# Kernel tuning notes

Hardware: AMD Instinct MI355X
Metric: run time of the kernel (lower is better)

The kernel has to match this reference:

```python
import jax, jax.numpy as jnp
import numpy as np

B, L, D, H = 2, 2048, 512, 8
DH = D // H
THRESHOLD = 0.1


def setup_inputs() -> dict:
    key = jax.random.key(0)
    ks = jax.random.split(key, 8)
    s = 0.02  # weight scale to keep activations sane
    return {
        "q_x": jax.random.normal(ks[0], (B, L, D), jnp.float32),
        "k_x": jax.random.normal(ks[1], (B, L, D), jnp.float32),
        "v_x": jax.random.normal(ks[2], (B, L, D), jnp.float32),
        "energy_coeffs": jax.random.normal(ks[3], (B, L, 16), jnp.float32),
        "Wq": jax.random.normal(ks[4], (D, D), jnp.float32) * s,
        "bq": jnp.zeros((D,), jnp.float32),
        "Wk": jax.random.normal(ks[5], (D, D), jnp.float32) * s,
        "bk": jnp.zeros((D,), jnp.float32),
        "Wv": jax.random.normal(ks[6], (D, D), jnp.float32) * s,
        "bv": jnp.zeros((D,), jnp.float32),
        "Wo": jax.random.normal(ks[7], (D, D), jnp.float32) * s,
        "bo": jnp.zeros((D,), jnp.float32),
    }


def reference(q_x, k_x, v_x, energy_coeffs, Wq, bq, Wk, bk, Wv, bv, Wo, bo):
    b, l, d = q_x.shape
    # QKV projections (torch Linear: x @ W.T + b), split heads -> [B,H,L,Dh]
    Q = (q_x @ Wq.T + bq).reshape(b, l, H, DH).transpose(0, 2, 1, 3)
    K = (k_x @ Wk.T + bk).reshape(b, -1, H, DH).transpose(0, 2, 1, 3)
    V = (v_x @ Wv.T + bv).reshape(b, -1, H, DH).transpose(0, 2, 1, 3)
    scores = jnp.einsum("bhqd,bhkd->bhqk", Q, K) / jnp.sqrt(jnp.float32(DH))
    # straight-through energy-based key mask
    energy = jnp.abs(energy_coeffs).mean(axis=-1)  # [B, Lk]
    soft = jax.nn.sigmoid((energy - THRESHOLD) * 10.0)
    hard = (energy > THRESHOLD).astype(q_x.dtype)
    mask_val = soft + jax.lax.stop_gradient(hard - soft)  # fwd=hard, grad=soft
    scores = scores + (1.0 - mask_val)[:, None, None, :] * (-1e9)
    attn = jax.nn.softmax(scores, axis=-1)
    out = jnp.einsum("bhqk,bhkd->bhqd", attn, V)
    out = out.transpose(0, 2, 1, 3).reshape(b, l, d)
    return out @ Wo.T + bo
```

## Files before the change

kernel.cpp:

```cpp
#include <hip/hip_runtime.h>
#include <stdint.h>

#define B_ 2
#define L_ 2048
#define D_ 512
#define H_ 8
#define DH_ 64

using frag8 = __attribute__((ext_vector_type(8))) short;
using bf4   = __attribute__((ext_vector_type(4))) short;
using f32x4 = __attribute__((ext_vector_type(4))) float;
using u32x4 = __attribute__((ext_vector_type(4))) unsigned int;

#define QSC 0.18033688011112042f

__device__ __forceinline__ unsigned short f2bf(float f) {
    unsigned int u = __float_as_uint(f);
    u += 0x7fffu + ((u >> 16) & 1u);
    return (unsigned short)(u >> 16);
}

__device__ __forceinline__ unsigned int cvtpk(float lo, float hi_) {
    unsigned int r;
    asm("v_cvt_pk_bf16_f32 %0, %1, %2" : "=v"(r) : "v"(lo), "v"(hi_));
    return r;
}

__device__ __forceinline__ void gl2lds16(const void* g, void* lds) {
    __builtin_amdgcn_global_load_lds((const __attribute__((address_space(1))) void*)g,
                                     (__attribute__((address_space(3))) void*)lds,
                                     16, 0, 0);
}

template<int N>
__device__ __forceinline__ void vmwait() {
    asm volatile("s_waitcnt vmcnt(%0)" :: "n"(N) : "memory");
}

__global__ __launch_bounds__(256) void cvt_mask_kernel(
    const float* __restrict__ qx, const float* __restrict__ kx, const float* __restrict__ vx,
    const float* __restrict__ Wq, const float* __restrict__ Wk, const float* __restrict__ Wv,
    const float* __restrict__ Wo, const float* __restrict__ ec,
    unsigned short* qb, unsigned short* kb, unsigned short* vb,
    unsigned short* wqb, unsigned short* wkb, unsigned short* wvb, unsigned short* wob,
    float* __restrict__ mk)
{
    const long NA = (long)B_ * L_ * D_;
    const long NW = (long)D_ * D_;
    const long total4 = (3 * NA + 4 * NW) / 4;
    long q4 = (long)blockIdx.x * 256 + threadIdx.x;
    if (q4 < total4) {
        long i = q4 * 4;
        const float* src; unsigned short* dst; long off;
        if (i < NA)            { src = qx; dst = qb; off = i; }
        else if (i < 2 * NA)   { src = kx; dst = kb; off = i - NA; }
        else if (i < 3 * NA)   { src = vx; dst = vb; off = i - 2 * NA; }
        else {
            long j = i - 3 * NA;
            int w = (int)(j / NW);
            off = j - (long)w * NW;
            src = (w == 0) ? Wq : (w == 1) ? Wk : (w == 2) ? Wv : Wo;
            dst = (w == 0) ? wqb : (w == 1) ? wkb : (w == 2) ? wvb : wob;
        }
        float4 v = *(const float4*)(src + off);
        ushort4 o;
        o.x = f2bf(v.x); o.y = f2bf(v.y); o.z = f2bf(v.z); o.w = f2bf(v.w);
        *(ushort4*)(dst + off) = o;
    } else {
        long i = q4 - total4;
        if (i < B_ * L_) {
            const float4* p4 = (const float4*)(ec + i * 16);
            float s = 0.0f;
#pragma unroll
            for (int j = 0; j < 4; ++j) {
                float4 v = p4[j];
                s += fabsf(v.x) + fabsf(v.y) + fabsf(v.z) + fabsf(v.w);
            }
            float energy = s * (1.0f / 16.0f);
            mk[i] = (energy > 0.1f) ? 0.0f : -1.0e9f;
        }
    }
}

struct GemmArgs { const unsigned short* A; const unsigned short* W;
                  const float* bias; void* C; int mode; };

template<int BM, int BN>
__global__ __launch_bounds__(256) void gemm_kernel(GemmArgs a0, GemmArgs a1, GemmArgs a2,
                                                   int M, int N, int K)
{
    const int nwg = gridDim.x * gridDim.y * gridDim.z;
    int flat = blockIdx.x + gridDim.x * (blockIdx.y + gridDim.y * blockIdx.z);
    int swz  = (flat & 7) * (nwg >> 3) + (flat >> 3);
    const int bx = swz % gridDim.x;
    int t2 = swz / gridDim.x;
    const int by = t2 % gridDim.y;
    const int bz = t2 / gridDim.y;

    GemmArgs ga = bz == 0 ? a0 : (bz == 1 ? a1 : a2);
    const unsigned short* __restrict__ A = ga.A;
    const unsigned short* __restrict__ W = ga.W;
    const float* __restrict__ bias = ga.bias;

    constexpr int MF = BM / 32;
    constexpr int NF = BN / 32;
    constexpr int NL = BM / 32 + BN / 32;

    __shared__ __align__(16) unsigned short As[2][BM * 64];
    __shared__ __align__(16) unsigned short Bs[2][BN * 64];

    const int tid  = threadIdx.x;
    const int lane = tid & 63;
    const int wave = tid >> 6;
    const int hi   = lane >> 4;
    const int ln   = lane & 15;
    const int wr   = wave >> 1;
    const int wc   = wave & 1;

    const long mBase = (long)by * BM;
    const long nBase = (long)bx * BN;

    f32x4 acc[MF][NF];
#pragma unroll
    for (int m = 0; m < MF; ++m)
#pragma unroll
        for (int n = 0; n < NF; ++n) acc[m][n] = (f32x4){0.f, 0.f, 0.f, 0.f};

#define GSTAGE(KT, BUF) do {                                                    \
    _Pragma("unroll")                                                           \
    for (int i_ = 0; i_ < BM / 32; ++i_) {                                      \
        int cl_ = i_ * 256 + tid;                                               \
        int r_ = cl_ >> 3, c_ = cl_ & 7, s_ = c_ ^ (r_ & 7);                    \
        gl2lds16(A + (mBase + r_) * K + (KT) + s_ * 8, As[BUF] + cl_ * 8);      \
    }                                                                           \
    _Pragma("unroll")                                                           \
    for (int i_ = 0; i_ < BN / 32; ++i_) {                                      \
        int cl_ = i_ * 256 + tid;                                               \
        int r_ = cl_ >> 3, c_ = cl_ & 7, s_ = c_ ^ (r_ & 7);                    \
        gl2lds16(W + (nBase + r_) * K + (KT) + s_ * 8, Bs[BUF] + cl_ * 8);      \
    }                                                                           \
} while (0)

    GSTAGE(0, 0);

    const int nk = K / 64;
    for (int t = 0; t < nk; ++t) {
        const int buf = t & 1;
        if (t + 1 < nk) {
            GSTAGE((t + 1) * 64, buf ^ 1);
            vmwait<NL>();
        } else {
            vmwait<0>();
        }
        __builtin_amdgcn_s_barrier();
        __builtin_amdgcn_sched_barrier(0);

        frag8 af[2][MF], bfr[2][NF];
#pragma unroll
        for (int kk = 0; kk < 2; ++kk) {
#pragma unroll
            for (int m = 0; m < MF; ++m) {
                int row = wr * (BM / 2) + m * 16 + ln;
                int c = (kk * 4 + hi) ^ (row & 7);
                af[kk][m] = *(const frag8*)(As[buf] + row * 64 + c * 8);
            }
#pragma unroll
            for (int n = 0; n < NF; ++n) {
                int row = wc * (BN / 2) + n * 16 + ln;
                int c = (kk * 4 + hi) ^ (row & 7);
                bfr[kk][n] = *(const frag8*)(Bs[buf] + row * 64 + c * 8);
            }
        }
        __builtin_amdgcn_s_setprio(1);
#pragma unroll
        for (int kk = 0; kk < 2; ++kk)
#pragma unroll
            for (int m = 0; m < MF; ++m)
#pragma unroll
                for (int n = 0; n < NF; ++n)
                    acc[m][n] = __builtin_amdgcn_mfma_f32_16x16x32_bf16(af[kk][m], bfr[kk][n], acc[m][n], 0, 0, 0);
        __builtin_amdgcn_s_setprio(0);
        __builtin_amdgcn_sched_barrier(0);
        __builtin_amdgcn_s_barrier();
    }
#undef GSTAGE

    const int mode = ga.mode;
#pragma unroll
    for (int m = 0; m < MF; ++m) {
#pragma unroll
        for (int n = 0; n < NF; ++n) {
            long col = nBase + wc * (BN / 2) + n * 16 + ln;
            float bv = bias[col];
#pragma unroll
            for (int j = 0; j < 4; ++j) {
                long row = mBase + wr * (BM / 2) + m * 16 + hi * 4 + j;
                float v = acc[m][n][j] + bv;
                if (mode == 3) {
                    ((float*)ga.C)[row * N + col] = v;
                } else if (mode == 2) {
                    int dh = (int)col & 63;
                    int swv = ((dh & 7) << 1) | ((dh >> 3) & 1);
                    long nt = (row & ~63L) | (long)(((((int)(row >> 2)) & 15) ^ swv) << 2) | (row & 3);
                    ((unsigned short*)ga.C)[col * (long)(B_ * L_) + nt] = f2bf(v);
                } else {
                    if (mode == 1) v *= QSC;
                    ((unsigned short*)ga.C)[row * N + col] = f2bf(v);
                }
            }
        }
    }
}

__global__ __launch_bounds__(512, 4) void attn_kernel(
    const unsigned short* __restrict__ Qg, const unsigned short* __restrict__ Kg,
    const unsigned short* __restrict__ Vt, const float* __restrict__ mkg,
    unsigned short* __restrict__ Og)
{
    const int tid  = threadIdx.x;
    const int lane = tid & 63;
    const int wave = tid >> 6;
    const int grp  = wave >> 2;
    const int wq   = wave & 3;
    const int gtid = tid & 255;
    const int hi   = lane >> 4;
    const int ln   = lane & 15;

    const int bh = blockIdx.y;
    const int b  = bh >> 3, h = bh & 7;
    const unsigned short* Qb = Qg + ((long)b * L_) * D_ + h * DH_;
    const unsigned short* Kb = Kg + ((long)b * L_) * D_ + h * DH_;
    const unsigned short* Vb = Vt + (long)(h * DH_) * (B_ * L_) + (long)b * L_;
    const float* mkb = mkg + (long)b * L_;

    __shared__ __align__(16) char smem[65536];
    unsigned short* KsG = (unsigned short*)(smem + grp * 32768);
    unsigned short* VsG = (unsigned short*)(smem + grp * 32768 + 16384);

    const int q0 = blockIdx.x * 64 + wq * 16;

    frag8 qf[2];
#pragma unroll
    for (int ks = 0; ks < 2; ++ks)
        qf[ks] = *(const frag8*)(Qb + (long)(q0 + ln) * D_ + ks * 32 + hi * 8);

    const int sw  = ((ln & 7) << 1) | ((ln >> 3) & 1);
    const int sl0 = ((hi     ) ^ sw) << 2;
    const int sl1 = ((hi + 4 ) ^ sw) << 2;
    const int sl2 = ((hi + 8 ) ^ sw) << 2;
    const int sl3 = ((hi + 12) ^ sw) << 2;

#define STAGE(TT, BUF) do {                                                     \
    _Pragma("unroll")                                                           \
    for (int c2_ = 0; c2_ < 2; ++c2_) {                                         \
        int cl_ = c2_ * 256 + gtid;                                             \
        int r_ = cl_ >> 3, c_ = cl_ & 7;                                        \
        gl2lds16(Kb + (long)((TT) * 64 + r_) * D_ + ((c_ ^ (r_ & 7)) << 3),     \
                 KsG + (BUF) * 4096 + cl_ * 8);                                 \
        gl2lds16(Vb + (long)r_ * (B_ * L_) + (TT) * 64 + (c_ << 3),             \
                 VsG + (BUF) * 4096 + cl_ * 8);                                 \
    }                                                                           \
} while (0)

    STAGE(grp, 0);

    f32x4 o[4];
#pragma unroll
    for (int g = 0; g < 4; ++g) o[g] = (f32x4){0.f, 0.f, 0.f, 0.f};
    float m_run = -__builtin_inff();
    float l_run = 0.0f;

    for (int i = 0; i < 16; ++i) {
        const int T = 2 * i + grp;
        const int buf = i & 1;

        float4 m40 = *(const float4*)(mkb + T * 64 +      4 * hi);
        float4 m41 = *(const float4*)(mkb + T * 64 + 16 + 4 * hi);
        float4 m42 = *(const float4*)(mkb + T * 64 + 32 + 4 * hi);
        float4 m43 = *(const float4*)(mkb + T * 64 + 48 + 4 * hi);
        __builtin_amdgcn_sched_barrier(0);

        if (i < 15) {
            STAGE(2 * (i + 1) + grp, buf ^ 1);
            vmwait<8>();
        } else {
            vmwait<4>();
        }
        __builtin_amdgcn_s_barrier();
        __builtin_amdgcn_sched_barrier(0);

        const unsigned short* Kl = KsG + buf * 4096;
        const unsigned short* Vl = VsG + buf * 4096;

        f32x4 sv[4];
#pragma unroll
        for (int sh = 0; sh < 4; ++sh) sv[sh] = (f32x4){0.f, 0.f, 0.f, 0.f};
        __builtin_amdgcn_s_setprio(1);
#pragma unroll
        for (int sh = 0; sh < 4; ++sh) {
            int key = sh * 16 + ln;
#pragma unroll
            for (int ks = 0; ks < 2; ++ks) {
                frag8 kf = *(const frag8*)(Kl + key * 64 + (((ks * 4 + hi) ^ (ln & 7)) << 3));
                sv[sh] = __builtin_amdgcn_mfma_f32_16x16x32_bf16(kf, qf[ks], sv[sh], 0, 0, 0);
            }
        }
        __builtin_amdgcn_s_setprio(0);

        float sc[16];
        sc[0]  = sv[0][0] + m40.x; sc[1]  = sv[0][1] + m40.y;
        sc[2]  = sv[0][2] + m40.z; sc[3]  = sv[0][3] + m40.w;
        sc[4]  = sv[1][0] + m41.x; sc[5]  = sv[1][1] + m41.y;
        sc[6]  = sv[1][2] + m41.z; sc[7]  = sv[1][3] + m41.w;
        sc[8]  = sv[2][0] + m42.x; sc[9]  = sv[2][1] + m42.y;
        sc[10] = sv[2][2] + m42.z; sc[11] = sv[2][3] + m42.w;
        sc[12] = sv[3][0] + m43.x; sc[13] = sv[3][1] + m43.y;
        sc[14] = sv[3][2] + m43.z; sc[15] = sv[3][3] + m43.w;

        float t0 = fmaxf(fmaxf(sc[0], sc[1]), sc[2]);
        float t1 = fmaxf(fmaxf(sc[3], sc[4]), sc[5]);
        float t2 = fmaxf(fmaxf(sc[6], sc[7]), sc[8]);
        float t3 = fmaxf(fmaxf(sc[9], sc[10]), sc[11]);
        float t4 = fmaxf(fmaxf(sc[12], sc[13]), sc[14]);
        float tmax = fmaxf(fmaxf(fmaxf(t0, t1), fmaxf(t2, t3)), fmaxf(t4, sc[15]));
        tmax = fmaxf(tmax, __shfl_xor(tmax, 16));
        tmax = fmaxf(tmax, __shfl_xor(tmax, 32));

        if (!__all(tmax <= m_run)) {
            float m_new = fmaxf(m_run, tmax);
            float alpha = __builtin_amdgcn_exp2f(m_run - m_new);
            float a0 = __shfl(alpha, 4 * hi + 0);
            float a1 = __shfl(alpha, 4 * hi + 1);
            float a2 = __shfl(alpha, 4 * hi + 2);
            float a3 = __shfl(alpha, 4 * hi + 3);
#pragma unroll
            for (int g = 0; g < 4; ++g) {
                o[g][0] *= a0; o[g][1] *= a1; o[g][2] *= a2; o[g][3] *= a3;
            }
            l_run *= alpha;
            m_run = m_new;
        }

        float p[16];
#pragma unroll
        for (int j = 0; j < 16; ++j) p[j] = __builtin_amdgcn_exp2f(sc[j] - m_run);
        float s01 = (p[0] + p[1]) + (p[2] + p[3]);
        float s23 = (p[4] + p[5]) + (p[6] + p[7]);
        float s45 = (p[8] + p[9]) + (p[10] + p[11]);
        float s67 = (p[12] + p[13]) + (p[14] + p[15]);
        float ps = (s01 + s23) + (s45 + s67);
        ps += __shfl_xor(ps, 16);
        ps += __shfl_xor(ps, 32);
        l_run += ps;

        union PU { u32x4 u; frag8 f; } p0u, p1u;
        p0u.u = (u32x4){cvtpk(p[0], p[1]),  cvtpk(p[2], p[3]),
                        cvtpk(p[4], p[5]),  cvtpk(p[6], p[7])};
        p1u.u = (u32x4){cvtpk(p[8], p[9]),  cvtpk(p[10], p[11]),
                        cvtpk(p[12], p[13]), cvtpk(p[14], p[15])};

        __builtin_amdgcn_s_setprio(1);
#pragma unroll
        for (int g = 0; g < 4; ++g) {
            int rowb = (g * 16 + ln) * 64;
            bf4 a0 = *(const bf4*)(Vl + rowb + sl0);
            bf4 a1 = *(const bf4*)(Vl + rowb + sl1);
            bf4 a2 = *(const bf4*)(Vl + rowb + sl2);
            bf4 a3 = *(const bf4*)(Vl + rowb + sl3);
            frag8 vf0 = __builtin_shufflevector(a0, a1, 0, 1, 2, 3, 4, 5, 6, 7);
            frag8 vf1 = __builtin_shufflevector(a2, a3, 0, 1, 2, 3, 4, 5, 6, 7);
            o[g] = __builtin_amdgcn_mfma_f32_16x16x32_bf16(p0u.f, vf0, o[g], 0, 0, 0);
            o[g] = __builtin_amdgcn_mfma_f32_16x16x32_bf16(p1u.f, vf1, o[g], 0, 0, 0);
        }
        __builtin_amdgcn_s_setprio(0);

        __builtin_amdgcn_sched_barrier(0);
        __builtin_amdgcn_s_barrier();
    }
#undef STAGE

    float* oX = (float*)smem;
    float* mX = (float*)(smem + 64 * 68 * 4);
    float* lX = mX + 64;

    if (grp == 1) {
#pragma unroll
        for (int g = 0; g < 4; ++g)
#pragma unroll
            for (int j = 0; j < 4; ++j)
                oX[(wq * 16 + 4 * hi + j) * 68 + g * 16 + ln] = o[g][j];
        if (hi == 0) { mX[wq * 16 + ln] = m_run; lX[wq * 16 + ln] = l_run; }
    }
    __syncthreads();
    if (grp == 0) {
#pragma unroll
        for (int j = 0; j < 4; ++j) {
            int q = 4 * hi + j;
            float mA = __shfl(m_run, q);
            float lA = __shfl(l_run, q);
            float mB = mX[wq * 16 + q];
            float lB = lX[wq * 16 + q];
            float mm = fmaxf(mA, mB);
            float aA = __builtin_amdgcn_exp2f(mA - mm);
            float aB = __builtin_amdgcn_exp2f(mB - mm);
            float inv = 1.0f / (lA * aA + lB * aB);
            aA *= inv; aB *= inv;
#pragma unroll
            for (int g = 0; g < 4; ++g) {
                float v = o[g][j] * aA + oX[(wq * 16 + q) * 68 + g * 16 + ln] * aB;
                long idx = ((long)b * L_ + q0 + q) * D_ + h * DH_ + g * 16 + ln;
                Og[idx] = f2bf(v);
            }
        }
    }
}

extern "C" void kernel_launch(void* const* d_in, const int* in_sizes, int n_in,
                              void* d_out, int out_size, void* d_ws, size_t ws_size,
                              hipStream_t stream)
{
    const float* qx = (const float*)d_in[0];
    const float* kx = (const float*)d_in[1];
    const float* vx = (const float*)d_in[2];
    const float* ec = (const float*)d_in[3];
    const float* Wq = (const float*)d_in[4];
    const float* bq = (const float*)d_in[5];
    const float* Wk = (const float*)d_in[6];
    const float* bk = (const float*)d_in[7];
    const float* Wv = (const float*)d_in[8];
    const float* bv = (const float*)d_in[9];
    const float* Wo = (const float*)d_in[10];
    const float* bo = (const float*)d_in[11];
    float* out = (float*)d_out;

    const long NA = (long)B_ * L_ * D_;
    const long NW = (long)D_ * D_;

    unsigned short* qb  = (unsigned short*)d_ws;
    unsigned short* kb  = qb + NA;
    unsigned short* vb  = kb + NA;
    unsigned short* wqb = vb + NA;
    unsigned short* wkb = wqb + NW;
    unsigned short* wvb = wkb + NW;
    unsigned short* wob = wvb + NW;
    unsigned short* Qp  = wob + NW;
    unsigned short* Kp  = Qp + NA;
    unsigned short* Vtp = Kp + NA;
    unsigned short* Ap  = qb;
    float*          mk  = (float*)(Vtp + NA);

    const long total4 = (3 * NA + 4 * NW) / 4;
    const long nblk = (total4 + B_ * L_ + 255) / 256;
    cvt_mask_kernel<<<dim3((unsigned)nblk), dim3(256), 0, stream>>>(
        qx, kx, vx, Wq, Wk, Wv, Wo, ec, qb, kb, vb, wqb, wkb, wvb, wob, mk);

    GemmArgs zq = {qb, wqb, bq, Qp, 1};
    GemmArgs zk = {kb, wkb, bk, Kp, 0};
    GemmArgs zv = {vb, wvb, bv, Vtp, 2};
    gemm_kernel<64, 128><<<dim3(4, 64, 3), dim3(256), 0, stream>>>(zq, zk, zv, B_ * L_, D_, D_);

    attn_kernel<<<dim3(L_ / 64, B_ * H_), dim3(512), 0, stream>>>(Qp, Kp, Vtp, mk, Ap);

    GemmArgs zo = {Ap, wob, bo, out, 3};
    gemm_kernel<64, 64><<<dim3(8, 64, 1), dim3(256), 0, stream>>>(zo, zo, zo, B_ * L_, D_, D_);
}
```

Baseline: 79.43 us.

## Fuse fp32-to-bf16 activation conversion into QKV GEMM and tune attention inner loop

The QKV projection GEMM now reads fp32 activations directly, converts them to bf16 in registers and writes them into swizzled LDS. This removes the separate conversion pass over the three activation tensors and its bf16 round trip through memory. The V-transpose swizzle is also changed so the attention kernel can load V fragments with single 16-byte LDS reads instead of four 8-byte reads. In addition, the attention loop gets unroll 2, butterfly reductions with three parallel shuffles, and a lazy rescale that only updates the running max when it grows by more than 8. The trade-offs are that the fp32 A path loses the async global-to-LDS copy and adds register pressure, and the lazy-rescale threshold could overflow in rare cases.

```diff
diff --git a/kernel.cpp b/kernel.cpp
--- a/kernel.cpp
+++ b/kernel.cpp
@@ -8,7 +8,6 @@
 #define DH_ 64
 
 using frag8 = __attribute__((ext_vector_type(8))) short;
-using bf4   = __attribute__((ext_vector_type(4))) short;
 using f32x4 = __attribute__((ext_vector_type(4))) float;
 using u32x4 = __attribute__((ext_vector_type(4))) unsigned int;
 
@@ -37,37 +36,30 @@
     asm volatile("s_waitcnt vmcnt(%0)" :: "n"(N) : "memory");
 }
 
+__device__ __forceinline__ void lgkmwait0() {
+    asm volatile("s_waitcnt lgkmcnt(0)" ::: "memory");
+}
+
 __global__ __launch_bounds__(256) void cvt_mask_kernel(
-    const float* __restrict__ qx, const float* __restrict__ kx, const float* __restrict__ vx,
     const float* __restrict__ Wq, const float* __restrict__ Wk, const float* __restrict__ Wv,
     const float* __restrict__ Wo, const float* __restrict__ ec,
-    unsigned short* qb, unsigned short* kb, unsigned short* vb,
     unsigned short* wqb, unsigned short* wkb, unsigned short* wvb, unsigned short* wob,
     float* __restrict__ mk)
 {
-    const long NA = (long)B_ * L_ * D_;
     const long NW = (long)D_ * D_;
-    const long total4 = (3 * NA + 4 * NW) / 4;
     long q4 = (long)blockIdx.x * 256 + threadIdx.x;
-    if (q4 < total4) {
+    if (q4 < NW) {
         long i = q4 * 4;
-        const float* src; unsigned short* dst; long off;
-        if (i < NA)            { src = qx; dst = qb; off = i; }
-        else if (i < 2 * NA)   { src = kx; dst = kb; off = i - NA; }
-        else if (i < 3 * NA)   { src = vx; dst = vb; off = i - 2 * NA; }
-        else {
-            long j = i - 3 * NA;
-            int w = (int)(j / NW);
-            off = j - (long)w * NW;
-            src = (w == 0) ? Wq : (w == 1) ? Wk : (w == 2) ? Wv : Wo;
-            dst = (w == 0) ? wqb : (w == 1) ? wkb : (w == 2) ? wvb : wob;
-        }
+        int w = (int)(i / NW);
+        long off = i - (long)w * NW;
+        const float* src = (w == 0) ? Wq : (w == 1) ? Wk : (w == 2) ? Wv : Wo;
+        unsigned short* dst = (w == 0) ? wqb : (w == 1) ? wkb : (w == 2) ? wvb : wob;
         float4 v = *(const float4*)(src + off);
         ushort4 o;
         o.x = f2bf(v.x); o.y = f2bf(v.y); o.z = f2bf(v.z); o.w = f2bf(v.w);
         *(ushort4*)(dst + off) = o;
     } else {
-        long i = q4 - total4;
+        long i = q4 - NW;
         if (i < B_ * L_) {
             const float4* p4 = (const float4*)(ec + i * 16);
             float s = 0.0f;
@@ -82,10 +74,10 @@
     }
 }
 
-struct GemmArgs { const unsigned short* A; const unsigned short* W;
+struct GemmArgs { const void* A; const unsigned short* W;
                   const float* bias; void* C; int mode; };
 
-template<int BM, int BN>
+template<int BM, int BN, int AF32>
 __global__ __launch_bounds__(256) void gemm_kernel(GemmArgs a0, GemmArgs a1, GemmArgs a2,
                                                    int M, int N, int K)
 {
@@ -98,13 +90,13 @@
     const int bz = t2 / gridDim.y;
 
     GemmArgs ga = bz == 0 ? a0 : (bz == 1 ? a1 : a2);
-    const unsigned short* __restrict__ A = ga.A;
+    const float* __restrict__ Af = (const float*)ga.A;
+    const unsigned short* __restrict__ Ab = (const unsigned short*)ga.A;
     const unsigned short* __restrict__ W = ga.W;
     const float* __restrict__ bias = ga.bias;
 
     constexpr int MF = BM / 32;
     constexpr int NF = BN / 32;
-    constexpr int NL = BM / 32 + BN / 32;
 
     __shared__ __align__(16) unsigned short As[2][BM * 64];
     __shared__ __align__(16) unsigned short Bs[2][BN * 64];
@@ -120,19 +112,18 @@
     const long mBase = (long)by * BM;
     const long nBase = (long)bx * BN;
 
+    const int ar = tid >> 2;
+    const int at = tid & 3;
+    const int ac0 = (2 * at) ^ (ar & 7);
+    const int ac1 = (2 * at + 1) ^ (ar & 7);
+
     f32x4 acc[MF][NF];
 #pragma unroll
     for (int m = 0; m < MF; ++m)
 #pragma unroll
         for (int n = 0; n < NF; ++n) acc[m][n] = (f32x4){0.f, 0.f, 0.f, 0.f};
 
-#define GSTAGE(KT, BUF) do {                                                    \
-    _Pragma("unroll")                                                           \
-    for (int i_ = 0; i_ < BM / 32; ++i_) {                                      \
-        int cl_ = i_ * 256 + tid;                                               \
-        int r_ = cl_ >> 3, c_ = cl_ & 7, s_ = c_ ^ (r_ & 7);                    \
-        gl2lds16(A + (mBase + r_) * K + (KT) + s_ * 8, As[BUF] + cl_ * 8);      \
-    }                                                                           \
+#define WSTAGE(KT, BUF) do {                                                    \
     _Pragma("unroll")                                                           \
     for (int i_ = 0; i_ < BN / 32; ++i_) {                                      \
         int cl_ = i_ * 256 + tid;                                               \
@@ -141,14 +132,55 @@
     }                                                                           \
 } while (0)
 
-    GSTAGE(0, 0);
+#define ASTAGE_BF16(KT, BUF) do {                                               \
+    _Pragma("unroll")                                                           \
+    for (int i_ = 0; i_ < BM / 32; ++i_) {                                      \
+        int cl_ = i_ * 256 + tid;                                               \
+        int r_ = cl_ >> 3, c_ = cl_ & 7, s_ = c_ ^ (r_ & 7);                    \
+        gl2lds16(Ab + (mBase + r_) * K + (KT) + s_ * 8, As[BUF] + cl_ * 8);     \
+    }                                                                           \
+} while (0)
+
+#define ALOAD_F32(KT) do {                                                      \
+    const float* s_ = Af + (mBase + ar) * K + (KT) + at * 16;                   \
+    av0 = *(const float4*)(s_);      av1 = *(const float4*)(s_ + 4);            \
+    av2 = *(const float4*)(s_ + 8);  av3 = *(const float4*)(s_ + 12);           \
+} while (0)
+
+#define AWRITE_F32(BUF) do {                                                    \
+    u32x4 w0_ = (u32x4){cvtpk(av0.x, av0.y), cvtpk(av0.z, av0.w),               \
+                        cvtpk(av1.x, av1.y), cvtpk(av1.z, av1.w)};              \
+    u32x4 w1_ = (u32x4){cvtpk(av2.x, av2.y), cvtpk(av2.z, av2.w),               \
+                        cvtpk(av3.x, av3.y), cvtpk(av3.z, av3.w)};              \
+    *(u32x4*)(As[BUF] + ar * 64 + ac0 * 8) = w0_;                               \
+    *(u32x4*)(As[BUF] + ar * 64 + ac1 * 8) = w1_;                               \
+} while (0)
+
+    float4 av0, av1, av2, av3;
+
+    if (AF32) {
+        ALOAD_F32(0);
+        WSTAGE(0, 0);
+        AWRITE_F32(0);
+        lgkmwait0();
+    } else {
+        ASTAGE_BF16(0, 0);
+        WSTAGE(0, 0);
+    }
 
     const int nk = K / 64;
     for (int t = 0; t < nk; ++t) {
         const int buf = t & 1;
         if (t + 1 < nk) {
-            GSTAGE((t + 1) * 64, buf ^ 1);
-            vmwait<NL>();
+            if (AF32) {
+                ALOAD_F32((t + 1) * 64);
+                WSTAGE((t + 1) * 64, buf ^ 1);
+                vmwait<8>();
+            } else {
+                ASTAGE_BF16((t + 1) * 64, buf ^ 1);
+                WSTAGE((t + 1) * 64, buf ^ 1);
+                vmwait<BM / 32 + BN / 32>();
+            }
         } else {
             vmwait<0>();
         }
@@ -180,10 +212,18 @@
                 for (int n = 0; n < NF; ++n)
                     acc[m][n] = __builtin_amdgcn_mfma_f32_16x16x32_bf16(af[kk][m], bfr[kk][n], acc[m][n], 0, 0, 0);
         __builtin_amdgcn_s_setprio(0);
+
+        if (AF32 && t + 1 < nk) {
+            AWRITE_F32(buf ^ 1);
+            lgkmwait0();
+        }
         __builtin_amdgcn_sched_barrier(0);
         __builtin_amdgcn_s_barrier();
     }
-#undef GSTAGE
+#undef WSTAGE
+#undef ASTAGE_BF16
+#undef ALOAD_F32
+#undef AWRITE_F32
 
     const int mode = ga.mode;
 #pragma unroll
@@ -200,8 +240,10 @@
                     ((float*)ga.C)[row * N + col] = v;
                 } else if (mode == 2) {
                     int dh = (int)col & 63;
-                    int swv = ((dh & 7) << 1) | ((dh >> 3) & 1);
-                    long nt = (row & ~63L) | (long)(((((int)(row >> 2)) & 15) ^ swv) << 2) | (row & 3);
+                    int s  = ((int)row >> 2) & 15;
+                    int w  = (int)row & 3;
+                    int q  = ((((s & 3) << 2) | (s >> 2)) ^ ((dh & 7) << 1));
+                    long nt = (row & ~63L) | (long)(q << 2) | w;
                     ((unsigned short*)ga.C)[col * (long)(B_ * L_) + nt] = f2bf(v);
                 } else {
                     if (mode == 1) v *= QSC;
@@ -244,11 +286,9 @@
     for (int ks = 0; ks < 2; ++ks)
         qf[ks] = *(const frag8*)(Qb + (long)(q0 + ln) * D_ + ks * 32 + hi * 8);
 
-    const int sw  = ((ln & 7) << 1) | ((ln >> 3) & 1);
-    const int sl0 = ((hi     ) ^ sw) << 2;
-    const int sl1 = ((hi + 4 ) ^ sw) << 2;
-    const int sl2 = ((hi + 8 ) ^ sw) << 2;
-    const int sl3 = ((hi + 12) ^ sw) << 2;
+    const int xv   = (ln & 7) << 1;
+    const int off0 = (((hi << 2) ^ xv)) << 2;
+    const int off1 = off0 ^ 8;
 
 #define STAGE(TT, BUF) do {                                                     \
     _Pragma("unroll")                                                           \
@@ -270,6 +310,7 @@
     float m_run = -__builtin_inff();
     float l_run = 0.0f;
 
+#pragma unroll 2
     for (int i = 0; i < 16; ++i) {
         const int T = 2 * i + grp;
         const int buf = i & 1;
@@ -317,16 +358,17 @@
         sc[12] = sv[3][0] + m43.x; sc[13] = sv[3][1] + m43.y;
         sc[14] = sv[3][2] + m43.z; sc[15] = sv[3][3] + m43.w;
 
-        float t0 = fmaxf(fmaxf(sc[0], sc[1]), sc[2]);
-        float t1 = fmaxf(fmaxf(sc[3], sc[4]), sc[5]);
-        float t2 = fmaxf(fmaxf(sc[6], sc[7]), sc[8]);
-        float t3 = fmaxf(fmaxf(sc[9], sc[10]), sc[11]);
-        float t4 = fmaxf(fmaxf(sc[12], sc[13]), sc[14]);
-        float tmax = fmaxf(fmaxf(fmaxf(t0, t1), fmaxf(t2, t3)), fmaxf(t4, sc[15]));
-        tmax = fmaxf(tmax, __shfl_xor(tmax, 16));
-        tmax = fmaxf(tmax, __shfl_xor(tmax, 32));
-
-        if (!__all(tmax <= m_run)) {
+        float t0 = fmaxf(fmaxf(sc[0], sc[1]), fmaxf(sc[2], sc[3]));
+        float t1 = fmaxf(fmaxf(sc[4], sc[5]), fmaxf(sc[6], sc[7]));
+        float t2 = fmaxf(fmaxf(sc[8], sc[9]), fmaxf(sc[10], sc[11]));
+        float t3 = fmaxf(fmaxf(sc[12], sc[13]), fmaxf(sc[14], sc[15]));
+        float tl = fmaxf(fmaxf(t0, t1), fmaxf(t2, t3));
+        float tA = __shfl_xor(tl, 16);
+        float tB = __shfl_xor(tl, 32);
+        float tC = __shfl_xor(tl, 48);
+        float tmax = fmaxf(fmaxf(tl, tA), fmaxf(tB, tC));
+
+        if (!__all(tmax <= m_run + 8.0f)) {
             float m_new = fmaxf(m_run, tmax);
             float alpha = __builtin_amdgcn_exp2f(m_run - m_new);
             float a0 = __shfl(alpha, 4 * hi + 0);
@@ -349,9 +391,10 @@
         float s45 = (p[8] + p[9]) + (p[10] + p[11]);
         float s67 = (p[12] + p[13]) + (p[14] + p[15]);
         float ps = (s01 + s23) + (s45 + s67);
-        ps += __shfl_xor(ps, 16);
-        ps += __shfl_xor(ps, 32);
-        l_run += ps;
+        float pA = __shfl_xor(ps, 16);
+        float pB = __shfl_xor(ps, 32);
+        float pC = __shfl_xor(ps, 48);
+        l_run += (ps + pA) + (pB + pC);
 
         union PU { u32x4 u; frag8 f; } p0u, p1u;
         p0u.u = (u32x4){cvtpk(p[0], p[1]),  cvtpk(p[2], p[3]),
@@ -362,13 +405,9 @@
         __builtin_amdgcn_s_setprio(1);
 #pragma unroll
         for (int g = 0; g < 4; ++g) {
-            int rowb = (g * 16 + ln) * 64;
-            bf4 a0 = *(const bf4*)(Vl + rowb + sl0);
-            bf4 a1 = *(const bf4*)(Vl + rowb + sl1);
-            bf4 a2 = *(const bf4*)(Vl + rowb + sl2);
-            bf4 a3 = *(const bf4*)(Vl + rowb + sl3);
-            frag8 vf0 = __builtin_shufflevector(a0, a1, 0, 1, 2, 3, 4, 5, 6, 7);
-            frag8 vf1 = __builtin_shufflevector(a2, a3, 0, 1, 2, 3, 4, 5, 6, 7);
+            int base = (g * 16 + ln) * 64;
+            frag8 vf0 = *(const frag8*)(Vl + base + off0);
+            frag8 vf1 = *(const frag8*)(Vl + base + off1);
             o[g] = __builtin_amdgcn_mfma_f32_16x16x32_bf16(p0u.f, vf0, o[g], 0, 0, 0);
             o[g] = __builtin_amdgcn_mfma_f32_16x16x32_bf16(p1u.f, vf1, o[g], 0, 0, 0);
         }
@@ -436,31 +475,27 @@
     const long NA = (long)B_ * L_ * D_;
     const long NW = (long)D_ * D_;
 
-    unsigned short* qb  = (unsigned short*)d_ws;
-    unsigned short* kb  = qb + NA;
-    unsigned short* vb  = kb + NA;
-    unsigned short* wqb = vb + NA;
+    unsigned short* Ap  = (unsigned short*)d_ws;
+    unsigned short* wqb = Ap + NA;
     unsigned short* wkb = wqb + NW;
     unsigned short* wvb = wkb + NW;
     unsigned short* wob = wvb + NW;
     unsigned short* Qp  = wob + NW;
     unsigned short* Kp  = Qp + NA;
     unsigned short* Vtp = Kp + NA;
-    unsigned short* Ap  = qb;
     float*          mk  = (float*)(Vtp + NA);
 
-    const long total4 = (3 * NA + 4 * NW) / 4;
-    const long nblk = (total4 + B_ * L_ + 255) / 256;
+    const long nblk = (NW + B_ * L_ + 255) / 256;
     cvt_mask_kernel<<<dim3((unsigned)nblk), dim3(256), 0, stream>>>(
-        qx, kx, vx, Wq, Wk, Wv, Wo, ec, qb, kb, vb, wqb, wkb, wvb, wob, mk);
-
-    GemmArgs zq = {qb, wqb, bq, Qp, 1};
-    GemmArgs zk = {kb, wkb, bk, Kp, 0};
-    GemmArgs zv = {vb, wvb, bv, Vtp, 2};
-    gemm_kernel<64, 128><<<dim3(4, 64, 3), dim3(256), 0, stream>>>(zq, zk, zv, B_ * L_, D_, D_);
+        Wq, Wk, Wv, Wo, ec, wqb, wkb, wvb, wob, mk);
+
+    GemmArgs zq = {qx, wqb, bq, Qp, 1};
+    GemmArgs zk = {kx, wkb, bk, Kp, 0};
+    GemmArgs zv = {vx, wvb, bv, Vtp, 2};
+    gemm_kernel<64, 128, 1><<<dim3(4, 64, 3), dim3(256), 0, stream>>>(zq, zk, zv, B_ * L_, D_, D_);
 
     attn_kernel<<<dim3(L_ / 64, B_ * H_), dim3(512), 0, stream>>>(Qp, Kp, Vtp, mk, Ap);
 
     GemmArgs zo = {Ap, wob, bo, out, 3};
-    gemm_kernel<64, 64><<<dim3(8, 64, 1), dim3(256), 0, stream>>>(zo, zo, zo, B_ * L_, D_, D_);
-}
+    gemm_kernel<64, 64, 0><<<dim3(8, 64, 1), dim3(256), 0, stream>>>(zo, zo, zo, B_ * L_, D_, D_);
+}
```

Measured after the change: 80.93 us. About the same (+1.9%).
